# Optimization experiments

Measured on AMD Instinct MI355X. Metric: run time of the kernel, lower is better.

The kernel has to match this reference:

```python
import jax, jax.numpy as jnp
import numpy as np

B, S, D = 2, 2048, 2048
H, HK = 16, 4          # n_heads, n_kv_heads
DK = D // H            # 128
REP = H // HK


def setup_inputs() -> dict:
    key = jax.random.key(0)
    ks = jax.random.split(key, 9)
    x = jax.random.normal(ks[0], (B, S, D), dtype=jnp.float32)
    # RoPE tables: [max_seq_len, d_k/2]
    inv_freq = 1.0 / (10000.0 ** (jnp.arange(0, DK, 2, dtype=jnp.float32) / DK))
    t = jnp.arange(S, dtype=jnp.float32)
    freqs = jnp.outer(t, inv_freq)  # [S, DK/2]
    freqs_cos = jnp.cos(freqs)
    freqs_sin = jnp.sin(freqs)
    sc = 0.02
    return {
        "x": x,
        "freqs_cos": freqs_cos,
        "freqs_sin": freqs_sin,
        "wq_w": jax.random.normal(ks[1], (D, D), dtype=jnp.float32) * sc,
        "wq_b": jnp.zeros((D,), dtype=jnp.float32),
        "wk_w": jax.random.normal(ks[2], (HK * DK, D), dtype=jnp.float32) * sc,
        "wk_b": jnp.zeros((HK * DK,), dtype=jnp.float32),
        "wv_w": jax.random.normal(ks[3], (HK * DK, D), dtype=jnp.float32) * sc,
        "wv_b": jnp.zeros((HK * DK,), dtype=jnp.float32),
        "wo_w": jax.random.normal(ks[4], (D, D), dtype=jnp.float32) * sc,
        "wo_b": jnp.zeros((D,), dtype=jnp.float32),
    }


def _apply_rope(t, cos, sin):
    # t: [b, h, s, dk]; cos/sin: [1, 1, s, dk/2]; interleaved pairs (even=real, odd=imag)
    tr = t[..., 0::2]
    ti = t[..., 1::2]
    out_r = tr * cos - ti * sin
    out_i = tr * sin + ti * cos
    return jnp.stack([out_r, out_i], axis=-1).reshape(t.shape)


def reference(x, freqs_cos, freqs_sin, wq_w, wq_b, wk_w, wk_b, wv_w, wv_b, wo_w, wo_b):
    b, s, d = x.shape
    q = (x @ wq_w.T + wq_b).reshape(b, s, H, DK).transpose(0, 2, 1, 3)   # [b,H,s,dk]
    k = (x @ wk_w.T + wk_b).reshape(b, s, HK, DK).transpose(0, 2, 1, 3)  # [b,HK,s,dk]
    v = (x @ wv_w.T + wv_b).reshape(b, s, HK, DK).transpose(0, 2, 1, 3)

    cos = freqs_cos[:s][None, None]  # [1,1,s,dk/2]
    sin = freqs_sin[:s][None, None]
    q = _apply_rope(q, cos, sin)
    k = _apply_rope(k, cos, sin)

    # GQA: group q heads by kv head instead of materializing repeat_kv
    qg = q.reshape(b, HK, REP, s, DK)
    scores = jnp.einsum("bgrqd,bgkd->bgrqk", qg, k) / jnp.sqrt(jnp.float32(DK))
    causal = jnp.triu(jnp.full((s, s), -jnp.inf, dtype=scores.dtype), k=1)
    attn = jax.nn.softmax(scores + causal, axis=-1)  # dropout=0.0 -> no-op
    out = jnp.einsum("bgrqk,bgkd->bgrqd", attn, v)   # [b,HK,REP,s,dk]
    out = out.reshape(b, H, s, DK).transpose(0, 2, 1, 3).reshape(b, s, d)
    return out @ wo_w.T + wo_b
```

## Files before the change

kernel.cpp:

```cpp
#include <hip/hip_runtime.h>

#define BDIM 2
#define SDIM 2048
#define DDIM 2048
#define HQ 16
#define HKV 4
#define DKH 128
#define NKV 512
#define NQKV 3072
#define MROWS 4096

typedef __attribute__((ext_vector_type(8))) short bf16x8;
typedef __attribute__((ext_vector_type(4))) float f32x4;
typedef __attribute__((ext_vector_type(8))) unsigned short u16x8;
typedef __attribute__((ext_vector_type(4))) unsigned short u16x4;

#define AS1 __attribute__((address_space(1)))
#define AS3 __attribute__((address_space(3)))

__device__ __forceinline__ unsigned short f2bf(float f) {
    union { float f; unsigned int u; } v; v.f = f;
    unsigned int r = v.u + 0x7FFFu + ((v.u >> 16) & 1u);
    return (unsigned short)(r >> 16);
}
__device__ __forceinline__ float bf2f(unsigned short u) {
    union { unsigned int u; float f; } v; v.u = ((unsigned int)u) << 16;
    return v.f;
}
__device__ __forceinline__ unsigned int pack2bf(float a, float b) {
    return (unsigned int)f2bf(a) | ((unsigned int)f2bf(b) << 16);
}

#define NX   ((size_t)MROWS * DDIM)
#define NWQ  ((size_t)DDIM * DDIM)
#define NWKV ((size_t)NKV * DDIM)
#define CAST_BLOCKS 18432
__global__ void cast_all(const float* __restrict__ x, const float* __restrict__ wq,
                         const float* __restrict__ wk, const float* __restrict__ wv,
                         const float* __restrict__ wo, unsigned short* __restrict__ dst,
                         const float* __restrict__ qb, const float* __restrict__ kb,
                         const float* __restrict__ vb, float* __restrict__ b3) {
    if (blockIdx.x >= CAST_BLOCKS) {
        int i = (blockIdx.x - CAST_BLOCKS) * 256 + threadIdx.x;
        if (i < DDIM) b3[i] = qb[i];
        else if (i < DDIM + NKV) b3[i] = kb[i - DDIM];
        else if (i < NQKV) b3[i] = vb[i - DDIM - NKV];
        return;
    }
    size_t i = ((size_t)blockIdx.x * blockDim.x + threadIdx.x) * 4;
    const size_t N0 = NX, N1 = N0 + NWQ, N2 = N1 + NWKV, N3 = N2 + NWKV;
    const float* src; size_t off;
    if (i < N0)      { src = x;  off = i; }
    else if (i < N1) { src = wq; off = i - N0; }
    else if (i < N2) { src = wk; off = i - N1; }
    else if (i < N3) { src = wv; off = i - N2; }
    else             { src = wo; off = i - N3; }
    float4 v = *(const float4*)(src + off);
    u16x4 o;
    o[0] = f2bf(v.x); o[1] = f2bf(v.y); o[2] = f2bf(v.z); o[3] = f2bf(v.w);
    *(u16x4*)(dst + i) = o;
}

__global__ void rope_trans(unsigned short* __restrict__ buf,
                           const float* __restrict__ cosT, const float* __restrict__ sinT,
                           unsigned short* __restrict__ Vt, float qscale) {
    if (blockIdx.x < MROWS) {
        int r = blockIdx.x, pos = r & (SDIM - 1);
        int col0 = threadIdx.x * 8;
        unsigned short* p = buf + (size_t)r * NQKV + col0;
        int i0 = (col0 & 127) >> 1;
        float4 c4 = *(const float4*)(cosT + pos * 64 + i0);
        float4 s4 = *(const float4*)(sinT + pos * 64 + i0);
        float sc = (col0 < DDIM) ? qscale : 1.f;
        u16x8 v = *(const u16x8*)p;
        u16x8 o;
        float cc[4] = {c4.x, c4.y, c4.z, c4.w}, ss[4] = {s4.x, s4.y, s4.z, s4.w};
#pragma unroll
        for (int k = 0; k < 4; ++k) {
            float xr = bf2f(v[2 * k]), xi = bf2f(v[2 * k + 1]);
            o[2 * k]     = f2bf((xr * cc[k] - xi * ss[k]) * sc);
            o[2 * k + 1] = f2bf((xr * ss[k] + xi * cc[k]) * sc);
        }
        *(u16x8*)p = o;
    } else {
        __shared__ unsigned short T[32][33];
        if (threadIdx.x >= 256) return;
        int t = blockIdx.x - MROWS;
        int s0 = (t & 63) * 32, d0 = ((t >> 6) & 15) * 32, b = t >> 10;
        int c = threadIdx.x & 31, r4 = threadIdx.x >> 5;
        for (int rr = r4; rr < 32; rr += 8)
            T[rr][c] = buf[(size_t)(b * SDIM + s0 + rr) * NQKV + (DDIM + NKV) + d0 + c];
        __syncthreads();
        int cp = ((c & 0x0C) << 1) | ((c & 0x10) >> 2) | (c & 3);
        for (int rr = r4; rr < 32; rr += 8)
            Vt[(size_t)(b * NKV + d0 + rr) * SDIM + s0 + cp] = T[c][rr];
    }
}

template <int BF16OUT, int BM, int BN, int WM, int WN>
__global__ __launch_bounds__(512, 2) void gemm8(
    const unsigned short* __restrict__ A,
    const unsigned short* __restrict__ Bm,
    const float* __restrict__ bias,
    void* __restrict__ Cv,
    int pitch, int Kdim) {
    constexpr int MF = BM / WM / 16;
    constexpr int NFRAG = BN / WN / 16;
    constexpr int AH = BM / 128;
    constexpr int BH = BN / 128;
    constexpr int AHR = BM / 2;
    constexpr int BHR = BN / 2;

    __shared__ unsigned short As[2][2][AHR * 64];
    __shared__ unsigned short Bs[2][2][BHR * 64];

    const int tid = threadIdx.x;
    const int lane = tid & 63;
    const int wid = tid >> 6;
    const int ml = lane & 15, quad = lane >> 4;
    const int wm = wid / WN, wn = wid % WN;
    const int bhf = wn / (WN / 2);
    const int brb = (wn % (WN / 2)) * (BN / WN);

    const int gx = gridDim.x;
    const int nwg = gx * gridDim.y;
    int w0 = blockIdx.y * gx + blockIdx.x;
    int wsw = (nwg & 7) ? w0 : ((w0 & 7) * (nwg >> 3) + (w0 >> 3));
    const int m0 = (wsw / gx) * BM, n0 = (wsw % gx) * BN;

    const int NT = Kdim >> 6;
    const int xr = ml & 7;

    const int sr = tid >> 3;
    const int sk = ((tid & 7) ^ (sr & 7)) * 8;
    const unsigned short* Ag0 = A + (size_t)(m0 + sr) * Kdim + sk;
    const unsigned short* Bg0 = Bm + (size_t)(n0 + sr) * Kdim + sk;

    f32x4 acc[MF][NFRAG] = {};

#define STG_A(bf, hf, kt)                                                                       \
    do {                                                                                        \
        _Pragma("unroll")                                                                       \
        for (int ll = 0; ll < AH; ++ll)                                                         \
            __builtin_amdgcn_global_load_lds(                                                   \
                (const AS1 unsigned int*)(Ag0 + (size_t)((hf) * AHR + ll * 64) * Kdim + (kt)),  \
                (AS3 unsigned int*)(&As[bf][hf][ll * 4096 + tid * 8]), 16, 0, 0);               \
    } while (0)
#define STG_B(bf, hf, kt)                                                                       \
    do {                                                                                        \
        _Pragma("unroll")                                                                       \
        for (int ll = 0; ll < BH; ++ll)                                                         \
            __builtin_amdgcn_global_load_lds(                                                   \
                (const AS1 unsigned int*)(Bg0 + (size_t)((hf) * BHR + ll * 64) * Kdim + (kt)),  \
                (AS3 unsigned int*)(&Bs[bf][hf][ll * 4096 + tid * 8]), 16, 0, 0);               \
    } while (0)
#define WAIT_VM_STEADY()                                                                        \
    do {                                                                                        \
        if constexpr (BH == 1)      asm volatile("s_waitcnt vmcnt(2)" ::: "memory");            \
        else if constexpr (BH == 2) asm volatile("s_waitcnt vmcnt(4)" ::: "memory");            \
        else                        asm volatile("s_waitcnt vmcnt(6)" ::: "memory");            \
    } while (0)

    STG_B(0, 0, 0); STG_B(0, 1, 0);
    STG_A(0, 0, 0); STG_A(0, 1, 0);
    if (NT > 1) {
        STG_B(1, 0, 64); STG_B(1, 1, 64);
        WAIT_VM_STEADY();
    } else {
        asm volatile("s_waitcnt vmcnt(0)" ::: "memory");
    }
    __builtin_amdgcn_s_barrier();
    __builtin_amdgcn_sched_barrier(0);

    for (int G = 0; G < NT; ++G) {
        const int cur = G & 1, nxt = cur ^ 1;
        const int ktA = (G + 1) * 64, ktB = (G + 2) * 64;
        const unsigned short* Bh = Bs[cur][bhf];

        bf16x8 bfr[NFRAG][2];
#pragma unroll
        for (int nj = 0; nj < NFRAG; ++nj)
#pragma unroll
            for (int kk = 0; kk < 2; ++kk)
                bfr[nj][kk] = *(const bf16x8*)&Bh[(brb + nj * 16 + ml) * 64 + ((kk * 4 + quad) ^ xr) * 8];

        bf16x8 af[MF][2];
#pragma unroll
        for (int mf = 0; mf < MF; ++mf) {
            const int arow0 = wm * (BM / WM) + mf * 16;
            const int ahf = arow0 / AHR;
            const int arin = arow0 % AHR + ml;
#pragma unroll
            for (int kk = 0; kk < 2; ++kk)
                af[mf][kk] = *(const bf16x8*)&As[cur][ahf][arin * 64 + ((kk * 4 + quad) ^ xr) * 8];
        }

        if (G + 1 < NT) { STG_A(nxt, 0, ktA); STG_A(nxt, 1, ktA); }

        __builtin_amdgcn_s_setprio(1);
#pragma unroll
        for (int kk = 0; kk < 2; ++kk)
#pragma unroll
            for (int mf = 0; mf < MF; ++mf)
#pragma unroll
                for (int nj = 0; nj < NFRAG; ++nj)
                    acc[mf][nj] = __builtin_amdgcn_mfma_f32_16x16x32_bf16(
                        af[mf][kk], bfr[nj][kk], acc[mf][nj], 0, 0, 0);
        __builtin_amdgcn_s_setprio(0);

        asm volatile("s_waitcnt lgkmcnt(0)" ::: "memory");
        __builtin_amdgcn_sched_barrier(0);
        __builtin_amdgcn_s_barrier();

        if (G + 2 < NT) { STG_B(cur, 0, ktB); STG_B(cur, 1, ktB); }
        if (G < NT - 2)       { WAIT_VM_STEADY(); }
        else if (G == NT - 2) { asm volatile("s_waitcnt vmcnt(0)" ::: "memory"); }
        __builtin_amdgcn_sched_barrier(0);
        __builtin_amdgcn_s_barrier();
        __builtin_amdgcn_sched_barrier(0);
    }
#undef STG_A
#undef STG_B
#undef WAIT_VM_STEADY

#pragma unroll
    for (int nj = 0; nj < NFRAG; ++nj) {
        const int col = n0 + wn * (BN / WN) + nj * 16 + ml;
        const float bj = bias[col];
#pragma unroll
        for (int mf = 0; mf < MF; ++mf) {
            const int row0 = m0 + wm * (BM / WM) + mf * 16 + quad * 4;
#pragma unroll
            for (int rr = 0; rr < 4; ++rr) {
                float v = acc[mf][nj][rr] + bj;
                if (BF16OUT)
                    ((unsigned short*)Cv)[(size_t)(row0 + rr) * pitch + col] = f2bf(v);
                else
                    ((float*)Cv)[(size_t)(row0 + rr) * pitch + col] = v;
            }
        }
    }
}

__global__ __launch_bounds__(256, 2) void attn_fwd(
    const unsigned short* __restrict__ Qp,
    const unsigned short* __restrict__ Kp,
    const unsigned short* __restrict__ Vt,
    unsigned short* __restrict__ O) {
    const int l = blockIdx.x;
    const int j = l & 15;
    const int h = (l >> 4) & 15;
    const int b = l >> 8;
    const int g = h >> 2;
    const int jh = 31 - j;
    const int tid = threadIdx.x;
    const int w = tid >> 6, lane = tid & 63;
    const int ml = lane & 15, quad = lane >> 4;
    const int rsub = lane >> 2, seg = lane & 3;
    const int pr = w >> 1;
    const int wsub = w & 1;

    __shared__ unsigned short Ks[2][4 * 64 * 32];
    __shared__ unsigned short Vs[2][2 * 128 * 32];

    int myqt = pr ? j : jh;
    int q0 = myqt * 64 + wsub * 32;

    bf16x8 aq[2][4];
    auto load_q = [&](int qt) {
#pragma unroll
        for (int g2 = 0; g2 < 2; ++g2) {
            const size_t qrow = (size_t)(b * SDIM + qt * 64 + wsub * 32 + g2 * 16 + ml);
#pragma unroll
            for (int kc = 0; kc < 4; ++kc)
                aq[g2][kc] = *(const bf16x8*)(Qp + qrow * NQKV + h * DKH + kc * 32 + quad * 8);
        }
    };
    load_q(myqt);

    f32x4 o_acc[2][8] = {};
    float l_acc[2] = {0.f, 0.f};

    auto store_out = [&](int qt) {
#pragma unroll
        for (int g2 = 0; g2 < 2; ++g2) {
            float lt = l_acc[g2];
            lt += __shfl_xor(lt, 16);
            lt += __shfl_xor(lt, 32);
            float inv = 1.f / lt;
            size_t rowbase = (size_t)(b * SDIM + qt * 64 + wsub * 32 + g2 * 16 + ml) * DDIM + h * DKH + quad * 4;
#pragma unroll
            for (int dt = 0; dt < 8; ++dt) {
                u16x4 ov;
#pragma unroll
                for (int r = 0; r < 4; ++r)
                    ov[r] = f2bf(o_acc[g2][dt][r] * inv);
                *(u16x4*)(O + rowbase + dt * 16) = ov;
            }
        }
    };

    for (int it = 0; it < 17; ++it) {
        int kt;
        if (pr == 0)       kt = it;
        else if (it <= j)  kt = it;
        else if (it <= 15) kt = 16 + it - j;
        else               kt = -1;

        __syncthreads();
        if (kt >= 0) {
            const int kb = kt * 64;
#pragma unroll
            for (int kc = 0; kc < 4; ++kc)
#pragma unroll
                for (int rh = 0; rh < 2; ++rh)
                    __builtin_amdgcn_global_load_lds(
                        (const AS1 unsigned int*)(Kp + (size_t)(b * SDIM + kb + rh * 32 + wsub * 16 + rsub) * NQKV + g * DKH + kc * 32 + seg * 8),
                        (AS3 unsigned int*)(&Ks[pr][kc * 2048 + rh * 1024 + wsub * 512 + lane * 8]), 16, 0, 0);
#pragma unroll
            for (int c = 0; c < 8; ++c) {
                int u = wsub * 8 + c, kc2 = u >> 3, rg = u & 7;
                __builtin_amdgcn_global_load_lds(
                    (const AS1 unsigned int*)(Vt + (size_t)(b * NKV + g * DKH + rg * 16 + rsub) * SDIM + kb + kc2 * 32 + seg * 8),
                    (AS3 unsigned int*)(&Vs[pr][u * 512 + lane * 8]), 16, 0, 0);
            }
        }
        __syncthreads();

        if (pr == 1 && it == j + 1) {
            store_out(j);
            myqt = jh; q0 = myqt * 64 + wsub * 32;
            load_q(jh);
#pragma unroll
            for (int g2 = 0; g2 < 2; ++g2) {
                l_acc[g2] = 0.f;
#pragma unroll
                for (int dt = 0; dt < 8; ++dt) o_acc[g2][dt] = (f32x4){0.f, 0.f, 0.f, 0.f};
            }
        }

        if (kt >= 0) {
            const int kb = kt * 64;
            __builtin_amdgcn_s_setprio(1);
            f32x4 st[2][4];
#pragma unroll
            for (int t = 0; t < 4; ++t) {
                bf16x8 ak[4];
#pragma unroll
                for (int kc = 0; kc < 4; ++kc)
                    ak[kc] = *(const bf16x8*)&Ks[pr][kc * 2048 + (t * 16 + ml) * 32 + quad * 8];
#pragma unroll
                for (int g2 = 0; g2 < 2; ++g2) {
                    f32x4 sc = {};
#pragma unroll
                    for (int kc = 0; kc < 4; ++kc)
                        sc = __builtin_amdgcn_mfma_f32_16x16x32_bf16(ak[kc], aq[g2][kc], sc, 0, 0, 0);
                    st[g2][t] = sc;
                }
            }

            if (kb + 63 > q0) {
#pragma unroll
                for (int g2 = 0; g2 < 2; ++g2) {
                    int qg = q0 + g2 * 16 + ml;
#pragma unroll
                    for (int t = 0; t < 4; ++t) {
                        int kvb = kb + t * 16 + quad * 4;
#pragma unroll
                        for (int r = 0; r < 4; ++r)
                            if (kvb + r > qg) st[g2][t][r] = -INFINITY;
                    }
                }
            }

            unsigned int pk[2][4][2];
#pragma unroll
            for (int g2 = 0; g2 < 2; ++g2) {
#pragma unroll
                for (int t = 0; t < 4; ++t) {
                    float p0 = __expf(st[g2][t][0] - 20.f);
                    float p1 = __expf(st[g2][t][1] - 20.f);
                    float p2 = __expf(st[g2][t][2] - 20.f);
                    float p3 = __expf(st[g2][t][3] - 20.f);
                    l_acc[g2] += (p0 + p1) + (p2 + p3);
                    pk[g2][t][0] = pack2bf(p0, p1);
                    pk[g2][t][1] = pack2bf(p2, p3);
                }
            }

#pragma unroll
            for (int c = 0; c < 2; ++c) {
                union { unsigned int u[4]; bf16x8 v; } pb[2];
#pragma unroll
                for (int g2 = 0; g2 < 2; ++g2) {
                    pb[g2].u[0] = pk[g2][2 * c][0];     pb[g2].u[1] = pk[g2][2 * c][1];
                    pb[g2].u[2] = pk[g2][2 * c + 1][0]; pb[g2].u[3] = pk[g2][2 * c + 1][1];
                }
#pragma unroll
                for (int dt = 0; dt < 8; ++dt) {
                    bf16x8 av = *(const bf16x8*)&Vs[pr][c * 4096 + (dt * 16 + ml) * 32 + quad * 8];
                    o_acc[0][dt] = __builtin_amdgcn_mfma_f32_16x16x32_bf16(av, pb[0].v, o_acc[0][dt], 0, 0, 0);
                    o_acc[1][dt] = __builtin_amdgcn_mfma_f32_16x16x32_bf16(av, pb[1].v, o_acc[1][dt], 0, 0, 0);
                }
            }
            __builtin_amdgcn_s_setprio(0);
        }
    }

    __syncthreads();
    float* Fo = (float*)&Ks[0][0];
    float* Fl = (float*)&Vs[0][0];
    if (pr == 0) {
#pragma unroll
        for (int g2 = 0; g2 < 2; ++g2) {
            Fl[(g2 * 2 + wsub) * 64 + lane] = l_acc[g2];
#pragma unroll
            for (int dt = 0; dt < 8; ++dt)
                *(f32x4*)&Fo[(g2 * 8 + dt) * 512 + wsub * 256 + lane * 4] = o_acc[g2][dt];
        }
    }
    __syncthreads();
    if (pr == 1) {
#pragma unroll
        for (int g2 = 0; g2 < 2; ++g2) {
            l_acc[g2] += Fl[(g2 * 2 + wsub) * 64 + lane];
#pragma unroll
            for (int dt = 0; dt < 8; ++dt) {
                f32x4 pa = *(const f32x4*)&Fo[(g2 * 8 + dt) * 512 + wsub * 256 + lane * 4];
#pragma unroll
                for (int r = 0; r < 4; ++r) o_acc[g2][dt][r] += pa[r];
            }
        }
        store_out(jh);
    }
}

extern "C" void kernel_launch(void* const* d_in, const int* in_sizes, int n_in,
                              void* d_out, int out_size, void* d_ws, size_t ws_size,
                              hipStream_t stream) {
    const float* x    = (const float*)d_in[0];
    const float* fcos = (const float*)d_in[1];
    const float* fsin = (const float*)d_in[2];
    const float* wq_w = (const float*)d_in[3];
    const float* wq_b = (const float*)d_in[4];
    const float* wk_w = (const float*)d_in[5];
    const float* wk_b = (const float*)d_in[6];
    const float* wv_w = (const float*)d_in[7];
    const float* wv_b = (const float*)d_in[8];
    const float* wo_w = (const float*)d_in[9];
    const float* wo_b = (const float*)d_in[10];
    float* out = (float*)d_out;

    char* ws = (char*)d_ws;
    size_t off = 0;
    auto alloc = [&](size_t bytes) {
        char* p = ws + off;
        off += (bytes + 255) & ~(size_t)255;
        return p;
    };
    unsigned short* xb  = (unsigned short*)alloc(NX * 2);
    unsigned short* W3  = (unsigned short*)alloc((size_t)NQKV * DDIM * 2);
    unsigned short* wob = (unsigned short*)alloc(NWQ * 2);
    float* b3           = (float*)alloc((size_t)NQKV * 4);
    unsigned short* qkv = (unsigned short*)alloc((size_t)MROWS * NQKV * 2);
    unsigned short* Vt  = (unsigned short*)alloc((size_t)BDIM * NKV * SDIM * 2);
    unsigned short* att = (unsigned short*)alloc((size_t)MROWS * DDIM * 2);

    cast_all<<<dim3(CAST_BLOCKS + 12), dim3(256), 0, stream>>>(
        x, wq_w, wk_w, wv_w, wo_w, xb, wq_b, wk_b, wv_b, b3);

    gemm8<1, 128, 384, 1, 8><<<dim3(NQKV / 384, MROWS / 128), 512, 0, stream>>>(
        xb, W3, b3, qkv, NQKV, DDIM);

    const float scale = 0.08838834764831845f;
    rope_trans<<<dim3(MROWS + 2048), dim3(320), 0, stream>>>(qkv, fcos, fsin, Vt, scale);

    attn_fwd<<<dim3(512), dim3(256), 0, stream>>>(qkv, qkv + DDIM, Vt, att);

    gemm8<0, 256, 128, 2, 4><<<dim3(DDIM / 128, MROWS / 256), 512, 0, stream>>>(
        att, wob, wo_b, out, DDIM, DDIM);
}
```

Before: 294.7 us.

## Load GEMM B operand fragments directly from global memory, bypassing LDS

Shared-memory staging of the weight (B) tiles in the GEMM kernel is removed. Each wave now loads its B fragments straight from global memory into registers every K step, and one of the two barriers per iteration goes away. The output-projection launch also changes its wave layout from 2x4 to 4x2. This cuts LDS traffic and synchronisation, but global-load latency now sits directly in front of the MFMAs without prefetch, and in the 4x2 layout several waves fetch the same B rows redundantly.

After: 361.3 us. +22.6%, slower.

```diff
diff --git a/kernel.cpp b/kernel.cpp
--- a/kernel.cpp
+++ b/kernel.cpp
@@ -107,20 +107,15 @@
     constexpr int MF = BM / WM / 16;
     constexpr int NFRAG = BN / WN / 16;
     constexpr int AH = BM / 128;
-    constexpr int BH = BN / 128;
     constexpr int AHR = BM / 2;
-    constexpr int BHR = BN / 2;
 
     __shared__ unsigned short As[2][2][AHR * 64];
-    __shared__ unsigned short Bs[2][2][BHR * 64];
 
     const int tid = threadIdx.x;
     const int lane = tid & 63;
     const int wid = tid >> 6;
     const int ml = lane & 15, quad = lane >> 4;
     const int wm = wid / WN, wn = wid % WN;
-    const int bhf = wn / (WN / 2);
-    const int brb = (wn % (WN / 2)) * (BN / WN);
 
     const int gx = gridDim.x;
     const int nwg = gx * gridDim.y;
@@ -134,7 +129,8 @@
     const int sr = tid >> 3;
     const int sk = ((tid & 7) ^ (sr & 7)) * 8;
     const unsigned short* Ag0 = A + (size_t)(m0 + sr) * Kdim + sk;
-    const unsigned short* Bg0 = Bm + (size_t)(n0 + sr) * Kdim + sk;
+
+    const unsigned short* Bg = Bm + (size_t)(n0 + wn * (BN / WN) + ml) * Kdim + quad * 8;
 
     f32x4 acc[MF][NFRAG] = {};
 
@@ -146,43 +142,15 @@
                 (const AS1 unsigned int*)(Ag0 + (size_t)((hf) * AHR + ll * 64) * Kdim + (kt)),  \
                 (AS3 unsigned int*)(&As[bf][hf][ll * 4096 + tid * 8]), 16, 0, 0);               \
     } while (0)
-#define STG_B(bf, hf, kt)                                                                       \
-    do {                                                                                        \
-        _Pragma("unroll")                                                                       \
-        for (int ll = 0; ll < BH; ++ll)                                                         \
-            __builtin_amdgcn_global_load_lds(                                                   \
-                (const AS1 unsigned int*)(Bg0 + (size_t)((hf) * BHR + ll * 64) * Kdim + (kt)),  \
-                (AS3 unsigned int*)(&Bs[bf][hf][ll * 4096 + tid * 8]), 16, 0, 0);               \
-    } while (0)
-#define WAIT_VM_STEADY()                                                                        \
-    do {                                                                                        \
-        if constexpr (BH == 1)      asm volatile("s_waitcnt vmcnt(2)" ::: "memory");            \
-        else if constexpr (BH == 2) asm volatile("s_waitcnt vmcnt(4)" ::: "memory");            \
-        else                        asm volatile("s_waitcnt vmcnt(6)" ::: "memory");            \
-    } while (0)
-
-    STG_B(0, 0, 0); STG_B(0, 1, 0);
+
     STG_A(0, 0, 0); STG_A(0, 1, 0);
-    if (NT > 1) {
-        STG_B(1, 0, 64); STG_B(1, 1, 64);
-        WAIT_VM_STEADY();
-    } else {
-        asm volatile("s_waitcnt vmcnt(0)" ::: "memory");
-    }
+    asm volatile("s_waitcnt vmcnt(0)" ::: "memory");
     __builtin_amdgcn_s_barrier();
     __builtin_amdgcn_sched_barrier(0);
 
     for (int G = 0; G < NT; ++G) {
         const int cur = G & 1, nxt = cur ^ 1;
-        const int ktA = (G + 1) * 64, ktB = (G + 2) * 64;
-        const unsigned short* Bh = Bs[cur][bhf];
-
-        bf16x8 bfr[NFRAG][2];
-#pragma unroll
-        for (int nj = 0; nj < NFRAG; ++nj)
-#pragma unroll
-            for (int kk = 0; kk < 2; ++kk)
-                bfr[nj][kk] = *(const bf16x8*)&Bh[(brb + nj * 16 + ml) * 64 + ((kk * 4 + quad) ^ xr) * 8];
+        const int kt = G * 64, ktA = kt + 64;
 
         bf16x8 af[MF][2];
 #pragma unroll
@@ -195,6 +163,13 @@
                 af[mf][kk] = *(const bf16x8*)&As[cur][ahf][arin * 64 + ((kk * 4 + quad) ^ xr) * 8];
         }
 
+        bf16x8 bfr[NFRAG][2];
+#pragma unroll
+        for (int nj = 0; nj < NFRAG; ++nj)
+#pragma unroll
+            for (int kk = 0; kk < 2; ++kk)
+                bfr[nj][kk] = *(const bf16x8*)(Bg + (size_t)(nj * 16) * Kdim + kt + kk * 32);
+
         if (G + 1 < NT) { STG_A(nxt, 0, ktA); STG_A(nxt, 1, ktA); }
 
         __builtin_amdgcn_s_setprio(1);
@@ -208,20 +183,12 @@
                         af[mf][kk], bfr[nj][kk], acc[mf][nj], 0, 0, 0);
         __builtin_amdgcn_s_setprio(0);
 
-        asm volatile("s_waitcnt lgkmcnt(0)" ::: "memory");
-        __builtin_amdgcn_sched_barrier(0);
-        __builtin_amdgcn_s_barrier();
-
-        if (G + 2 < NT) { STG_B(cur, 0, ktB); STG_B(cur, 1, ktB); }
-        if (G < NT - 2)       { WAIT_VM_STEADY(); }
-        else if (G == NT - 2) { asm volatile("s_waitcnt vmcnt(0)" ::: "memory"); }
+        asm volatile("s_waitcnt vmcnt(0)" ::: "memory");
         __builtin_amdgcn_sched_barrier(0);
         __builtin_amdgcn_s_barrier();
         __builtin_amdgcn_sched_barrier(0);
     }
 #undef STG_A
-#undef STG_B
-#undef WAIT_VM_STEADY
 
 #pragma unroll
     for (int nj = 0; nj < NFRAG; ++nj) {
@@ -477,6 +444,6 @@
 
     attn_fwd<<<dim3(512), dim3(256), 0, stream>>>(qkv, qkv + DDIM, Vt, att);
 
-    gemm8<0, 256, 128, 2, 4><<<dim3(DDIM / 128, MROWS / 256), 512, 0, stream>>>(
+    gemm8<0, 256, 128, 4, 2><<<dim3(DDIM / 128, MROWS / 256), 512, 0, stream>>>(
         att, wob, wo_b, out, DDIM, DDIM);
 }
```

## Split QKV GEMM into four barrier phases and swizzle attention K/V LDS

Applied to the files above, without the earlier changes.

Adds a gemm4p variant for the QKV projection. Each K step is split into four phases that load A fragments in pairs, spread the next tile's global-to-LDS loads across the phases, and put a barrier around each MFMA group. The intent is to interleave memory traffic with compute more evenly. The attention kernel also gets an XOR swizzle on the K and V LDS layout, applied on both the load and read side, to cut bank conflicts. The extra barriers per K step add synchronization overhead, and gemm4p hardcodes 128 rows per warp, so it only works for that configuration.

Result: no change. 290.2 us (-1.5%).

```diff
diff --git a/kernel.cpp b/kernel.cpp
--- a/kernel.cpp
+++ b/kernel.cpp
@@ -98,13 +98,12 @@
 }
 
 template <int BF16OUT, int BM, int BN, int WM, int WN>
-__global__ __launch_bounds__(512, 2) void gemm8(
+__global__ __launch_bounds__(512, 2) void gemm4p(
     const unsigned short* __restrict__ A,
     const unsigned short* __restrict__ Bm,
     const float* __restrict__ bias,
     void* __restrict__ Cv,
     int pitch, int Kdim) {
-    constexpr int MF = BM / WM / 16;
     constexpr int NFRAG = BN / WN / 16;
     constexpr int AH = BM / 128;
     constexpr int BH = BN / 128;
@@ -136,7 +135,7 @@
     const unsigned short* Ag0 = A + (size_t)(m0 + sr) * Kdim + sk;
     const unsigned short* Bg0 = Bm + (size_t)(n0 + sr) * Kdim + sk;
 
-    f32x4 acc[MF][NFRAG] = {};
+    f32x4 acc[8][NFRAG] = {};
 
 #define STG_A(bf, hf, kt)                                                                       \
     do {                                                                                        \
@@ -170,6 +169,154 @@
         asm volatile("s_waitcnt vmcnt(0)" ::: "memory");
     }
     __builtin_amdgcn_s_barrier();
+
+    for (int G = 0; G < NT; ++G) {
+        const int cur = G & 1, nxt = cur ^ 1;
+        const int ktA = (G + 1) * 64, ktB = (G + 2) * 64;
+        const unsigned short* Bh = Bs[cur][bhf];
+
+        bf16x8 bfr[NFRAG][2];
+#pragma unroll
+        for (int nj = 0; nj < NFRAG; ++nj)
+#pragma unroll
+            for (int kk = 0; kk < 2; ++kk)
+                bfr[nj][kk] = *(const bf16x8*)&Bh[(brb + nj * 16 + ml) * 64 + ((kk * 4 + quad) ^ xr) * 8];
+
+#pragma unroll
+        for (int p = 0; p < 4; ++p) {
+            bf16x8 af[2][2];
+#pragma unroll
+            for (int mi = 0; mi < 2; ++mi) {
+                const int arow0 = wm * 128 + (p * 2 + mi) * 16;
+                const int ahf = arow0 / AHR;
+                const int arin = arow0 % AHR + ml;
+#pragma unroll
+                for (int kk = 0; kk < 2; ++kk)
+                    af[mi][kk] = *(const bf16x8*)&As[cur][ahf][arin * 64 + ((kk * 4 + quad) ^ xr) * 8];
+            }
+
+            if (p == 0) {
+                if (G + 1 < NT) { STG_A(nxt, 0, ktA); STG_A(nxt, 1, ktA); }
+            } else if (p == 2) {
+                if (G + 2 < NT) STG_B(cur, 0, ktB);
+            } else if (p == 3) {
+                if (G + 2 < NT) STG_B(cur, 1, ktB);
+            }
+
+            __builtin_amdgcn_s_barrier();
+            __builtin_amdgcn_s_setprio(1);
+#pragma unroll
+            for (int kk = 0; kk < 2; ++kk)
+#pragma unroll
+                for (int mi = 0; mi < 2; ++mi)
+#pragma unroll
+                    for (int nj = 0; nj < NFRAG; ++nj)
+                        acc[p * 2 + mi][nj] = __builtin_amdgcn_mfma_f32_16x16x32_bf16(
+                            af[mi][kk], bfr[nj][kk], acc[p * 2 + mi][nj], 0, 0, 0);
+            __builtin_amdgcn_s_setprio(0);
+            if (p == 3) {
+                if (G < NT - 2)       { WAIT_VM_STEADY(); }
+                else if (G == NT - 2) { asm volatile("s_waitcnt vmcnt(0)" ::: "memory"); }
+            }
+            __builtin_amdgcn_s_barrier();
+        }
+    }
+#undef STG_A
+#undef STG_B
+#undef WAIT_VM_STEADY
+
+#pragma unroll
+    for (int nj = 0; nj < NFRAG; ++nj) {
+        const int col = n0 + wn * (BN / WN) + nj * 16 + ml;
+        const float bj = bias[col];
+#pragma unroll
+        for (int mi = 0; mi < 8; ++mi) {
+            const int row0 = m0 + wm * 128 + mi * 16 + quad * 4;
+#pragma unroll
+            for (int rr = 0; rr < 4; ++rr) {
+                float v = acc[mi][nj][rr] + bj;
+                if (BF16OUT)
+                    ((unsigned short*)Cv)[(size_t)(row0 + rr) * pitch + col] = f2bf(v);
+                else
+                    ((float*)Cv)[(size_t)(row0 + rr) * pitch + col] = v;
+            }
+        }
+    }
+}
+
+template <int BF16OUT, int BM, int BN, int WM, int WN>
+__global__ __launch_bounds__(512, 2) void gemm2b(
+    const unsigned short* __restrict__ A,
+    const unsigned short* __restrict__ Bm,
+    const float* __restrict__ bias,
+    void* __restrict__ Cv,
+    int pitch, int Kdim) {
+    constexpr int MF = BM / WM / 16;
+    constexpr int NFRAG = BN / WN / 16;
+    constexpr int AH = BM / 128;
+    constexpr int BH = BN / 128;
+    constexpr int AHR = BM / 2;
+    constexpr int BHR = BN / 2;
+
+    __shared__ unsigned short As[2][2][AHR * 64];
+    __shared__ unsigned short Bs[2][2][BHR * 64];
+
+    const int tid = threadIdx.x;
+    const int lane = tid & 63;
+    const int wid = tid >> 6;
+    const int ml = lane & 15, quad = lane >> 4;
+    const int wm = wid / WN, wn = wid % WN;
+    const int bhf = wn / (WN / 2);
+    const int brb = (wn % (WN / 2)) * (BN / WN);
+
+    const int gx = gridDim.x;
+    const int nwg = gx * gridDim.y;
+    int w0 = blockIdx.y * gx + blockIdx.x;
+    int wsw = (nwg & 7) ? w0 : ((w0 & 7) * (nwg >> 3) + (w0 >> 3));
+    const int m0 = (wsw / gx) * BM, n0 = (wsw % gx) * BN;
+
+    const int NT = Kdim >> 6;
+    const int xr = ml & 7;
+
+    const int sr = tid >> 3;
+    const int sk = ((tid & 7) ^ (sr & 7)) * 8;
+    const unsigned short* Ag0 = A + (size_t)(m0 + sr) * Kdim + sk;
+    const unsigned short* Bg0 = Bm + (size_t)(n0 + sr) * Kdim + sk;
+
+    f32x4 acc[MF][NFRAG] = {};
+
+#define STG_A(bf, hf, kt)                                                                       \
+    do {                                                                                        \
+        _Pragma("unroll")                                                                       \
+        for (int ll = 0; ll < AH; ++ll)                                                         \
+            __builtin_amdgcn_global_load_lds(                                                   \
+                (const AS1 unsigned int*)(Ag0 + (size_t)((hf) * AHR + ll * 64) * Kdim + (kt)),  \
+                (AS3 unsigned int*)(&As[bf][hf][ll * 4096 + tid * 8]), 16, 0, 0);               \
+    } while (0)
+#define STG_B(bf, hf, kt)                                                                       \
+    do {                                                                                        \
+        _Pragma("unroll")                                                                       \
+        for (int ll = 0; ll < BH; ++ll)                                                         \
+            __builtin_amdgcn_global_load_lds(                                                   \
+                (const AS1 unsigned int*)(Bg0 + (size_t)((hf) * BHR + ll * 64) * Kdim + (kt)),  \
+                (AS3 unsigned int*)(&Bs[bf][hf][ll * 4096 + tid * 8]), 16, 0, 0);               \
+    } while (0)
+#define WAIT_VM_STEADY()                                                                        \
+    do {                                                                                        \
+        if constexpr (BH == 1)      asm volatile("s_waitcnt vmcnt(2)" ::: "memory");            \
+        else if constexpr (BH == 2) asm volatile("s_waitcnt vmcnt(4)" ::: "memory");            \
+        else                        asm volatile("s_waitcnt vmcnt(6)" ::: "memory");            \
+    } while (0)
+
+    STG_B(0, 0, 0); STG_B(0, 1, 0);
+    STG_A(0, 0, 0); STG_A(0, 1, 0);
+    if (NT > 1) {
+        STG_B(1, 0, 64); STG_B(1, 1, 64);
+        WAIT_VM_STEADY();
+    } else {
+        asm volatile("s_waitcnt vmcnt(0)" ::: "memory");
+    }
+    __builtin_amdgcn_s_barrier();
     __builtin_amdgcn_sched_barrier(0);
 
     for (int G = 0; G < NT; ++G) {
@@ -259,6 +406,8 @@
     const int rsub = lane >> 2, seg = lane & 3;
     const int pr = w >> 1;
     const int wsub = w & 1;
+    const int ssw = (rsub >> 1) & 3;
+    const int xsw = (ml >> 1) & 3;
 
     __shared__ unsigned short Ks[2][4 * 64 * 32];
     __shared__ unsigned short Vs[2][2 * 128 * 32];
@@ -315,13 +464,13 @@
 #pragma unroll
                 for (int rh = 0; rh < 2; ++rh)
                     __builtin_amdgcn_global_load_lds(
-                        (const AS1 unsigned int*)(Kp + (size_t)(b * SDIM + kb + rh * 32 + wsub * 16 + rsub) * NQKV + g * DKH + kc * 32 + seg * 8),
+                        (const AS1 unsigned int*)(Kp + (size_t)(b * SDIM + kb + rh * 32 + wsub * 16 + rsub) * NQKV + g * DKH + kc * 32 + (seg ^ ssw) * 8),
                         (AS3 unsigned int*)(&Ks[pr][kc * 2048 + rh * 1024 + wsub * 512 + lane * 8]), 16, 0, 0);
 #pragma unroll
             for (int c = 0; c < 8; ++c) {
                 int u = wsub * 8 + c, kc2 = u >> 3, rg = u & 7;
                 __builtin_amdgcn_global_load_lds(
-                    (const AS1 unsigned int*)(Vt + (size_t)(b * NKV + g * DKH + rg * 16 + rsub) * SDIM + kb + kc2 * 32 + seg * 8),
+                    (const AS1 unsigned int*)(Vt + (size_t)(b * NKV + g * DKH + rg * 16 + rsub) * SDIM + kb + kc2 * 32 + (seg ^ ssw) * 8),
                     (AS3 unsigned int*)(&Vs[pr][u * 512 + lane * 8]), 16, 0, 0);
             }
         }
@@ -348,7 +497,7 @@
                 bf16x8 ak[4];
 #pragma unroll
                 for (int kc = 0; kc < 4; ++kc)
-                    ak[kc] = *(const bf16x8*)&Ks[pr][kc * 2048 + (t * 16 + ml) * 32 + quad * 8];
+                    ak[kc] = *(const bf16x8*)&Ks[pr][kc * 2048 + (t * 16 + ml) * 32 + (quad ^ xsw) * 8];
 #pragma unroll
                 for (int g2 = 0; g2 < 2; ++g2) {
                     f32x4 sc = {};
@@ -398,7 +547,7 @@
                 }
 #pragma unroll
                 for (int dt = 0; dt < 8; ++dt) {
-                    bf16x8 av = *(const bf16x8*)&Vs[pr][c * 4096 + (dt * 16 + ml) * 32 + quad * 8];
+                    bf16x8 av = *(const bf16x8*)&Vs[pr][c * 4096 + (dt * 16 + ml) * 32 + (quad ^ xsw) * 8];
                     o_acc[0][dt] = __builtin_amdgcn_mfma_f32_16x16x32_bf16(av, pb[0].v, o_acc[0][dt], 0, 0, 0);
                     o_acc[1][dt] = __builtin_amdgcn_mfma_f32_16x16x32_bf16(av, pb[1].v, o_acc[1][dt], 0, 0, 0);
                 }
@@ -469,7 +618,7 @@
     cast_all<<<dim3(CAST_BLOCKS + 12), dim3(256), 0, stream>>>(
         x, wq_w, wk_w, wv_w, wo_w, xb, wq_b, wk_b, wv_b, b3);
 
-    gemm8<1, 128, 384, 1, 8><<<dim3(NQKV / 384, MROWS / 128), 512, 0, stream>>>(
+    gemm4p<1, 128, 384, 1, 8><<<dim3(NQKV / 384, MROWS / 128), 512, 0, stream>>>(
         xb, W3, b3, qkv, NQKV, DDIM);
 
     const float scale = 0.08838834764831845f;
@@ -477,6 +626,6 @@
 
     attn_fwd<<<dim3(512), dim3(256), 0, stream>>>(qkv, qkv + DDIM, Vt, att);
 
-    gemm8<0, 256, 128, 2, 4><<<dim3(DDIM / 128, MROWS / 256), 512, 0, stream>>>(
+    gemm2b<0, 256, 128, 2, 4><<<dim3(DDIM / 128, MROWS / 256), 512, 0, stream>>>(
         att, wob, wo_b, out, DDIM, DDIM);
 }
```
